# Kernel optimization log

Hardware: AMD Instinct MI355X
Metric: run time of the kernel (lower is better)

## Reference

```python
import jax, jax.numpy as jnp
import numpy as np

B, S, D, H = 2, 2048, 2048, 32
HD = D // H  # head_dim = 64
NEG = -1e10


def setup_inputs() -> dict:
    key = jax.random.key(0)
    k1, k2, k3 = jax.random.split(key, 3)
    hidden_states = jax.random.normal(k1, (B, S, D), dtype=jnp.float32)
    W = jax.random.normal(k2, (D, 3 * D), dtype=jnp.float32) * (1.0 / np.sqrt(D))
    b = jax.random.normal(k3, (3 * D,), dtype=jnp.float32) * 0.02
    return {"hidden_states": hidden_states, "W": W, "b": b}


def reference(hidden_states, W, b):
    # fused QKV projection: [B,S,D] @ [D,3D] -> [B,S,3D]
    qvk = hidden_states @ W + b
    # OPT interleaved layout: reshape to [B,S,D,3]; channel 0=q, 1=v, 2=k
    qvk = qvk.reshape(B, S, D, 3)
    q = qvk[..., 0].reshape(B, S, H, HD)
    v = qvk[..., 1].reshape(B, S, H, HD)
    k = qvk[..., 2].reshape(B, S, H, HD)
    # causal bias: -1e10 strictly above diagonal, shape [1,1,S,S]
    bias = jnp.triu(jnp.full((S, S), NEG, dtype=jnp.float32), 1)[None, None]
    # dot_product_attention_weights: scale q by 1/sqrt(head_dim)
    scale = jnp.asarray(1.0 / np.sqrt(HD), dtype=jnp.float32)
    scores = jnp.einsum('bqhd,bkhd->bhqk', q * scale, k) + bias  # [B,H,S,S]
    attn_weights = jax.nn.softmax(scores, axis=-1)
    attn_output = jnp.einsum('bhqk,bkhd->bqhd', attn_weights, v)  # [B,S,H,HD]
    return attn_output.reshape(B, S, D)
```

## Files before the change

kernel.cpp:

```cpp
#include <hip/hip_runtime.h>
#include <hip/hip_bf16.h>
#include <stdint.h>

typedef unsigned short ushort_t;
typedef __bf16 bf16x8 __attribute__((ext_vector_type(8)));
typedef float f32x4 __attribute__((ext_vector_type(4)));
typedef float f32x16 __attribute__((ext_vector_type(16)));
typedef int int4v __attribute__((ext_vector_type(4)));
typedef ushort_t ushort8 __attribute__((ext_vector_type(8)));

__device__ __forceinline__ ushort_t f2bf(float f) {
  union { float f; unsigned int u; } v; v.f = f;
  unsigned int r = v.u + 0x7fffu + ((v.u >> 16) & 1u);
  return (ushort_t)(r >> 16);
}

__device__ __forceinline__ bf16x8 ld_bf8(const ushort_t* p) {
  return *reinterpret_cast<const bf16x8*>(p);
}

__device__ __forceinline__ void g2lds16(const void* g, void* l) {
  __builtin_amdgcn_global_load_lds(
      (const __attribute__((address_space(1))) unsigned int*)g,
      (__attribute__((address_space(3))) unsigned int*)l,
      16, 0, 0);
}

__device__ __forceinline__ float ex2(float x) { return __builtin_amdgcn_exp2f(x); }

__device__ __forceinline__ int cvtpk(float a, float b) {
  int r;
  asm("v_cvt_pk_bf16_f32 %0, %1, %2" : "=v"(r) : "v"(a), "v"(b));
  return r;
}

__global__ __launch_bounds__(256) void cvt_hs(const float* __restrict__ in,
                                              ushort_t* __restrict__ out) {
  int i = (blockIdx.x * 256 + threadIdx.x) * 8;
  float4 a = *reinterpret_cast<const float4*>(in + i);
  float4 b = *reinterpret_cast<const float4*>(in + i + 4);
  ushort8 r;
  r[0] = f2bf(a.x); r[1] = f2bf(a.y); r[2] = f2bf(a.z); r[3] = f2bf(a.w);
  r[4] = f2bf(b.x); r[5] = f2bf(b.y); r[6] = f2bf(b.z); r[7] = f2bf(b.w);
  *reinterpret_cast<ushort8*>(out + i) = r;
}

__global__ __launch_bounds__(256) void transpose_W(const float* __restrict__ Win,
                                                   ushort_t* __restrict__ Wt) {
  __shared__ ushort_t T[64][65];
  const int t = threadIdx.x;
  const int k0 = (blockIdx.x & 31) * 64;
  const int n0 = (blockIdx.x >> 5) * 64;
#pragma unroll
  for (int i = 0; i < 16; ++i) {
    int idx = i * 256 + t;
    int r = idx >> 6, c = idx & 63;
    T[r][c] = f2bf(Win[(k0 + r) * 6144 + n0 + c]);
  }
  __syncthreads();
#pragma unroll
  for (int i = 0; i < 16; ++i) {
    int idx = i * 256 + t;
    int nr = idx >> 6, kc = idx & 63;
    Wt[(n0 + nr) * 2048 + k0 + kc] = T[kc][nr];
  }
}

__global__ __launch_bounds__(256, 2) void gemm_qkv(
    const ushort_t* __restrict__ A, const ushort_t* __restrict__ Bt,
    const float* __restrict__ bias,
    ushort_t* __restrict__ Qb, ushort_t* __restrict__ Kb,
    ushort_t* __restrict__ VT) {
  __shared__ __align__(16) char smem[40960];
  ushort_t* A0 = (ushort_t*)smem;
  ushort_t* A1 = (ushort_t*)(smem + 8192);
  ushort_t* B0 = (ushort_t*)(smem + 16384);
  ushort_t* B1 = (ushort_t*)(smem + 28672);
  ushort_t* Cs = (ushort_t*)smem;
  const int t = threadIdx.x;
  const int w = t >> 6, l = t & 63;
  const int lo = l & 15, hi = l >> 4;
  const int wr = w >> 1, wc = w & 1;

  int bid = blockIdx.x;
  int swz = (bid & 7) * 128 + (bid >> 3);
  const int mt = swz & 31, nt = swz >> 5;
  const int bm = mt * 128;
  const int bn = nt * 192;

  f32x4 acc[4][6];
#pragma unroll
  for (int i = 0; i < 4; ++i)
#pragma unroll
    for (int j = 0; j < 6; ++j) acc[i][j] = f32x4{0.f, 0.f, 0.f, 0.f};

  const ushort_t* Ag = A + (size_t)bm * 2048;
  const ushort_t* Bg = Bt + (size_t)bn * 2048;

#define STAGE(Ad, Bd, kk_)                                       \
  do {                                                           \
    for (int r2 = 0; r2 < 2; ++r2) {                             \
      int c_ = r2 * 256 + t;                                     \
      int row_ = c_ >> 2, s4_ = c_ & 3;                          \
      int slot_ = s4_ ^ ((row_ & 3) ^ ((row_ >> 2) & 3));        \
      g2lds16(Ag + row_ * 2048 + (kk_) + slot_ * 8, (Ad) + c_ * 8); \
    }                                                            \
    for (int r3 = 0; r3 < 3; ++r3) {                             \
      int c_ = r3 * 256 + t;                                     \
      int row_ = c_ >> 2, s4_ = c_ & 3;                          \
      int slot_ = s4_ ^ ((row_ & 3) ^ ((row_ >> 2) & 3));        \
      g2lds16(Bg + row_ * 2048 + (kk_) + slot_ * 8, (Bd) + c_ * 8); \
    }                                                            \
  } while (0)

  STAGE(A0, B0, 0);
  __syncthreads();
  ushort_t *Ac = A0, *Bc = B0, *An = A1, *Bn = B1;

  for (int kk = 0; kk < 2048; kk += 32) {
    if (kk + 32 < 2048) STAGE(An, Bn, kk + 32);
    bf16x8 af[4], bfr[6];
#pragma unroll
    for (int mf = 0; mf < 4; ++mf) {
      int row = wr * 64 + mf * 16 + lo;
      int fr = (row & 3) ^ ((row >> 2) & 3);
      af[mf] = ld_bf8(Ac + row * 32 + ((hi ^ fr) << 3));
    }
#pragma unroll
    for (int nf = 0; nf < 6; ++nf) {
      int row = wc * 96 + nf * 16 + lo;
      int fr = (row & 3) ^ ((row >> 2) & 3);
      bfr[nf] = ld_bf8(Bc + row * 32 + ((hi ^ fr) << 3));
    }
    __builtin_amdgcn_s_setprio(1);
#pragma unroll
    for (int mf = 0; mf < 4; ++mf)
#pragma unroll
      for (int nf = 0; nf < 6; ++nf)
        acc[mf][nf] = __builtin_amdgcn_mfma_f32_16x16x32_bf16(
            af[mf], bfr[nf], acc[mf][nf], 0, 0, 0);
    __builtin_amdgcn_s_setprio(0);
    __syncthreads();
    ushort_t* tmp;
    tmp = Ac; Ac = An; An = tmp;
    tmp = Bc; Bc = Bn; Bn = tmp;
  }
#undef STAGE

  float bv[6];
  int ch[6];
#pragma unroll
  for (int nf = 0; nf < 6; ++nf) {
    int nl = wc * 96 + nf * 16 + lo;
    bv[nf] = bias[bn + nl];
    ch[nf] = nl % 3;
  }
  const int b_ = bm >> 11;
  const int bh = (b_ << 5) + nt;
  const float QS = 0.125f * 1.44269504f;

#pragma unroll
  for (int h = 0; h < 2; ++h) {
    if (wr == h) {
#pragma unroll
      for (int mf = 0; mf < 4; ++mf)
#pragma unroll
        for (int nf = 0; nf < 6; ++nf) {
          int rloc = mf * 16 + hi * 4;
          int nl = wc * 96 + nf * 16 + lo;
          f32x4 a = acc[mf][nf];
#pragma unroll
          for (int j = 0; j < 4; ++j) {
            float v = a[j] + bv[nf];
            if (ch[nf] == 0) v *= QS;
            Cs[(rloc + j) * 200 + nl] = f2bf(v);
          }
        }
    }
    __syncthreads();
    const int sbase = (bm & 2047) + h * 64;
#pragma unroll
    for (int it = 0; it < 2; ++it) {
      int slot = it * 256 + t;
      int r = slot >> 3, g = slot & 7;
      ushort8 vq, vk;
#pragma unroll
      for (int u = 0; u < 8; ++u) {
        int hd = g * 8 + u;
        vq[u] = Cs[r * 200 + hd * 3];
        vk[u] = Cs[r * 200 + hd * 3 + 2];
      }
      size_t rowoff = ((size_t)bh * 2048 + sbase + r) * 64 + g * 8;
      *reinterpret_cast<ushort8*>(Qb + rowoff) = vq;
      *reinterpret_cast<ushort8*>(Kb + rowoff) = vk;
    }
#pragma unroll
    for (int it = 0; it < 2; ++it) {
      int slot = it * 256 + t;
      int hd = slot >> 3, sg = slot & 7;
      ushort8 vv;
#pragma unroll
      for (int u = 0; u < 8; ++u) vv[u] = Cs[(sg * 8 + u) * 200 + hd * 3 + 1];
      *reinterpret_cast<ushort8*>(VT + ((size_t)bh * 64 + hd) * 2048 + sbase +
                                  sg * 8) = vv;
    }
    __syncthreads();
  }
}

__global__ __launch_bounds__(64) void attn(
    const ushort_t* __restrict__ Qb, const ushort_t* __restrict__ Kb,
    const ushort_t* __restrict__ VT, float* __restrict__ out) {
  __shared__ float Ld[32 * 66];
  const int l = threadIdx.x;
  const int ql = l & 31, hi = l >> 5;

  const int bid = blockIdx.x;
  const int bh = bid & 63;
  const int qt = 63 - (bid >> 6);
  const int q0 = qt * 32;
  const int nch = qt + 1;

  const ushort_t* qp = Qb + (bh * 2048 + q0 + ql) * 64 + hi * 8;
  bf16x8 qf[4];
#pragma unroll
  for (int dc = 0; dc < 4; ++dc) qf[dc] = ld_bf8(qp + dc * 16);

  f32x16 o0, o1;
#pragma unroll
  for (int r = 0; r < 16; ++r) { o0[r] = 0.f; o1[r] = 0.f; }
  float mr = -1e30f, lr = 0.f;

  const ushort_t* kbase = Kb + bh * 2048 * 64 + hi * 8;
  const ushort_t* vbase = VT + (bh * 64 + ql) * 2048 + hi * 8;

  bf16x8 kf[4], vf0[2], vf1[2];
  {
    const ushort_t* kp = kbase + ql * 64;
#pragma unroll
    for (int dc = 0; dc < 4; ++dc) kf[dc] = ld_bf8(kp + dc * 16);
#pragma unroll
    for (int s = 0; s < 2; ++s) {
      const ushort_t* vp = vbase + s * 16;
      vf0[s] = ld_bf8(vp);
      vf1[s] = ld_bf8(vp + 32 * 2048);
    }
  }

  for (int c = 0; c < nch; ++c) {
    const int cn = (c + 1 < nch) ? (c + 1) : c;
    const ushort_t* kpn = kbase + (cn * 32 + ql) * 64;
    bf16x8 kn[4], vn0[2], vn1[2];
#pragma unroll
    for (int dc = 0; dc < 4; ++dc) kn[dc] = ld_bf8(kpn + dc * 16);
#pragma unroll
    for (int s = 0; s < 2; ++s) {
      const ushort_t* vpn = vbase + cn * 32 + s * 16;
      vn0[s] = ld_bf8(vpn);
      vn1[s] = ld_bf8(vpn + 32 * 2048);
    }

    f32x16 p;
#pragma unroll
    for (int r = 0; r < 16; ++r) p[r] = 0.f;
    __builtin_amdgcn_s_setprio(1);
#pragma unroll
    for (int dc = 0; dc < 4; ++dc)
      p = __builtin_amdgcn_mfma_f32_32x32x16_bf16(kf[dc], qf[dc], p, 0, 0, 0);
    __builtin_amdgcn_s_setprio(0);
    if (c == nch - 1) {
#pragma unroll
      for (int r = 0; r < 16; ++r) {
        int kvr = (r & 3) + 8 * (r >> 2) + 4 * hi;
        if (kvr > ql) p[r] = -1e30f;
      }
    }
    float a0 = fmaxf(p[0], p[1]), a1 = fmaxf(p[2], p[3]);
    float a2 = fmaxf(p[4], p[5]), a3 = fmaxf(p[6], p[7]);
    float a4 = fmaxf(p[8], p[9]), a5 = fmaxf(p[10], p[11]);
    float a6 = fmaxf(p[12], p[13]), a7 = fmaxf(p[14], p[15]);
    float mx = fmaxf(fmaxf(fmaxf(a0, a1), fmaxf(a2, a3)),
                     fmaxf(fmaxf(a4, a5), fmaxf(a6, a7)));
    if (__any(mx > mr + 10.0f)) {
      mx = fmaxf(mx, __shfl_xor(mx, 32));
      float mn = fmaxf(mr, mx);
      float scl = ex2(mr - mn);
      mr = mn;
      lr *= scl;
#pragma unroll
      for (int r = 0; r < 16; ++r) { o0[r] *= scl; o1[r] *= scl; }
    }
#pragma unroll
    for (int r = 0; r < 16; ++r) p[r] = ex2(p[r] - mr);
    float s0 = (p[0] + p[1]) + (p[2] + p[3]);
    float s1 = (p[4] + p[5]) + (p[6] + p[7]);
    float s2 = (p[8] + p[9]) + (p[10] + p[11]);
    float s3 = (p[12] + p[13]) + (p[14] + p[15]);
    lr += (s0 + s1) + (s2 + s3);

    __builtin_amdgcn_s_setprio(1);
#pragma unroll
    for (int s = 0; s < 2; ++s) {
      int x0 = cvtpk(p[8 * s + 0], p[8 * s + 1]);
      int x1 = cvtpk(p[8 * s + 2], p[8 * s + 3]);
      int y0 = cvtpk(p[8 * s + 4], p[8 * s + 5]);
      int y1 = cvtpk(p[8 * s + 6], p[8 * s + 7]);
      int ox0 = __shfl_xor(x0, 32);
      int ox1 = __shfl_xor(x1, 32);
      int oy0 = __shfl_xor(y0, 32);
      int oy1 = __shfl_xor(y1, 32);
      int4v wv;
      wv[0] = hi ? oy0 : x0;
      wv[1] = hi ? oy1 : x1;
      wv[2] = hi ? y0 : ox0;
      wv[3] = hi ? y1 : ox1;
      bf16x8 pf = __builtin_bit_cast(bf16x8, wv);
      o0 = __builtin_amdgcn_mfma_f32_32x32x16_bf16(vf0[s], pf, o0, 0, 0, 0);
      o1 = __builtin_amdgcn_mfma_f32_32x32x16_bf16(vf1[s], pf, o1, 0, 0, 0);
    }
    __builtin_amdgcn_s_setprio(0);
#pragma unroll
    for (int dc = 0; dc < 4; ++dc) kf[dc] = kn[dc];
#pragma unroll
    for (int s = 0; s < 2; ++s) {
      vf0[s] = vn0[s];
      vf1[s] = vn1[s];
    }
  }

  const float lrf = lr + __shfl_xor(lr, 32);
  const float inv = 1.0f / lrf;
#pragma unroll
  for (int r = 0; r < 16; ++r) {
    int hdv = (r & 3) + 8 * (r >> 2) + 4 * hi;
    Ld[ql * 66 + hdv] = o0[r] * inv;
    Ld[ql * 66 + 32 + hdv] = o1[r] * inv;
  }
  __syncthreads();
  const int b_ = bh >> 5, h = bh & 31;
  float* op = out + (size_t)(b_ * 2048 + q0) * 2048 + h * 64 + l;
#pragma unroll
  for (int i = 0; i < 32; ++i) {
    op[(size_t)i * 2048] = Ld[i * 66 + l];
  }
}

extern "C" void kernel_launch(void* const* d_in, const int* in_sizes, int n_in,
                              void* d_out, int out_size, void* d_ws,
                              size_t ws_size, hipStream_t stream) {
  (void)in_sizes; (void)n_in; (void)out_size; (void)ws_size;
  const float* hs = (const float*)d_in[0];
  const float* W = (const float*)d_in[1];
  const float* bias = (const float*)d_in[2];
  float* out = (float*)d_out;

  char* ws = (char*)d_ws;
  ushort_t* Abf = (ushort_t*)(ws);
  ushort_t* Wt = (ushort_t*)(ws + (16u << 20));
  ushort_t* Qb = (ushort_t*)(ws + (40u << 20));
  ushort_t* Kb = (ushort_t*)(ws + (56u << 20));
  ushort_t* VT = (ushort_t*)(ws + (72u << 20));

  hipLaunchKernelGGL(cvt_hs, dim3(4096), dim3(256), 0, stream, hs, Abf);
  hipLaunchKernelGGL(transpose_W, dim3(3072), dim3(256), 0, stream, W, Wt);
  hipLaunchKernelGGL(gemm_qkv, dim3(1024), dim3(256), 0, stream, Abf, Wt, bias,
                     Qb, Kb, VT);
  hipLaunchKernelGGL(attn, dim3(4096), dim3(64), 0, stream, Qb, Kb, VT, out);
}
```

Baseline: 263.4 us.

## Pair causal query tiles per block and double-buffer K/V loads in attention

Each attention block now processes two query tiles, pr and 63-pr, so every block does the same amount of causal work, and the grid is halved to 2048 blocks. The KV loop is unrolled by two with ping-pong register buffers (kA/kB). This removes the per-iteration register copies and the clamped redundant prefetch, and the diagonal mask now runs only on the last chunk. The cost is fewer blocks for latency hiding and tiles handled one after another inside a block. Register pressure may also rise from the doubled buffers.

After: 258.2 us. No clear change (-2.0%).

```diff
diff --git a/kernel.cpp b/kernel.cpp
--- a/kernel.cpp
+++ b/kernel.cpp
@@ -208,6 +208,84 @@
   }
 }
 
+__device__ __forceinline__ void ldkv(const ushort_t* kp, const ushort_t* vp,
+                                     bf16x8 k[4], bf16x8 v0[2], bf16x8 v1[2]) {
+#pragma unroll
+  for (int dc = 0; dc < 4; ++dc) k[dc] = ld_bf8(kp + dc * 16);
+#pragma unroll
+  for (int s = 0; s < 2; ++s) {
+    v0[s] = ld_bf8(vp + s * 16);
+    v1[s] = ld_bf8(vp + s * 16 + 32 * 2048);
+  }
+}
+
+__device__ __forceinline__ void proc_chunk(const bf16x8 kf[4],
+                                           const bf16x8 vf0[2],
+                                           const bf16x8 vf1[2],
+                                           const bf16x8 qf[4], f32x16& o0,
+                                           f32x16& o1, float& mr, float& lr,
+                                           bool diag, int ql, int hi) {
+  f32x16 p;
+#pragma unroll
+  for (int r = 0; r < 16; ++r) p[r] = 0.f;
+  __builtin_amdgcn_s_setprio(1);
+#pragma unroll
+  for (int dc = 0; dc < 4; ++dc)
+    p = __builtin_amdgcn_mfma_f32_32x32x16_bf16(kf[dc], qf[dc], p, 0, 0, 0);
+  __builtin_amdgcn_s_setprio(0);
+  if (diag) {
+#pragma unroll
+    for (int r = 0; r < 16; ++r) {
+      int kvr = (r & 3) + 8 * (r >> 2) + 4 * hi;
+      if (kvr > ql) p[r] = -1e30f;
+    }
+  }
+  float a0 = fmaxf(p[0], p[1]), a1 = fmaxf(p[2], p[3]);
+  float a2 = fmaxf(p[4], p[5]), a3 = fmaxf(p[6], p[7]);
+  float a4 = fmaxf(p[8], p[9]), a5 = fmaxf(p[10], p[11]);
+  float a6 = fmaxf(p[12], p[13]), a7 = fmaxf(p[14], p[15]);
+  float mx = fmaxf(fmaxf(fmaxf(a0, a1), fmaxf(a2, a3)),
+                   fmaxf(fmaxf(a4, a5), fmaxf(a6, a7)));
+  if (__any(mx > mr + 10.0f)) {
+    mx = fmaxf(mx, __shfl_xor(mx, 32));
+    float mn = fmaxf(mr, mx);
+    float scl = ex2(mr - mn);
+    mr = mn;
+    lr *= scl;
+#pragma unroll
+    for (int r = 0; r < 16; ++r) { o0[r] *= scl; o1[r] *= scl; }
+  }
+#pragma unroll
+  for (int r = 0; r < 16; ++r) p[r] = ex2(p[r] - mr);
+  float s0 = (p[0] + p[1]) + (p[2] + p[3]);
+  float s1 = (p[4] + p[5]) + (p[6] + p[7]);
+  float s2 = (p[8] + p[9]) + (p[10] + p[11]);
+  float s3 = (p[12] + p[13]) + (p[14] + p[15]);
+  lr += (s0 + s1) + (s2 + s3);
+
+  __builtin_amdgcn_s_setprio(1);
+#pragma unroll
+  for (int s = 0; s < 2; ++s) {
+    int x0 = cvtpk(p[8 * s + 0], p[8 * s + 1]);
+    int x1 = cvtpk(p[8 * s + 2], p[8 * s + 3]);
+    int y0 = cvtpk(p[8 * s + 4], p[8 * s + 5]);
+    int y1 = cvtpk(p[8 * s + 6], p[8 * s + 7]);
+    int ox0 = __shfl_xor(x0, 32);
+    int ox1 = __shfl_xor(x1, 32);
+    int oy0 = __shfl_xor(y0, 32);
+    int oy1 = __shfl_xor(y1, 32);
+    int4v wv;
+    wv[0] = hi ? oy0 : x0;
+    wv[1] = hi ? oy1 : x1;
+    wv[2] = hi ? y0 : ox0;
+    wv[3] = hi ? y1 : ox1;
+    bf16x8 pf = __builtin_bit_cast(bf16x8, wv);
+    o0 = __builtin_amdgcn_mfma_f32_32x32x16_bf16(vf0[s], pf, o0, 0, 0, 0);
+    o1 = __builtin_amdgcn_mfma_f32_32x32x16_bf16(vf1[s], pf, o1, 0, 0, 0);
+  }
+  __builtin_amdgcn_s_setprio(0);
+}
+
 __global__ __launch_bounds__(64) void attn(
     const ushort_t* __restrict__ Qb, const ushort_t* __restrict__ Kb,
     const ushort_t* __restrict__ VT, float* __restrict__ out) {
@@ -217,131 +295,66 @@
 
   const int bid = blockIdx.x;
   const int bh = bid & 63;
-  const int qt = 63 - (bid >> 6);
-  const int q0 = qt * 32;
-  const int nch = qt + 1;
-
-  const ushort_t* qp = Qb + (bh * 2048 + q0 + ql) * 64 + hi * 8;
-  bf16x8 qf[4];
-#pragma unroll
-  for (int dc = 0; dc < 4; ++dc) qf[dc] = ld_bf8(qp + dc * 16);
-
-  f32x16 o0, o1;
-#pragma unroll
-  for (int r = 0; r < 16; ++r) { o0[r] = 0.f; o1[r] = 0.f; }
-  float mr = -1e30f, lr = 0.f;
+  const int pr = bid >> 6;
+  const int b_ = bh >> 5, h = bh & 31;
 
   const ushort_t* kbase = Kb + bh * 2048 * 64 + hi * 8;
   const ushort_t* vbase = VT + (bh * 64 + ql) * 2048 + hi * 8;
-
-  bf16x8 kf[4], vf0[2], vf1[2];
-  {
+  const int KSTR = 32 * 64;
+  const int VSTR = 32;
+
+#pragma unroll 1
+  for (int tile = 0; tile < 2; ++tile) {
+    const int qt = tile ? (63 - pr) : pr;
+    const int q0 = qt * 32;
+    const int nch = qt + 1;
+
+    const ushort_t* qp = Qb + (bh * 2048 + q0 + ql) * 64 + hi * 8;
+    bf16x8 qf[4];
+#pragma unroll
+    for (int dc = 0; dc < 4; ++dc) qf[dc] = ld_bf8(qp + dc * 16);
+
+    f32x16 o0, o1;
+#pragma unroll
+    for (int r = 0; r < 16; ++r) { o0[r] = 0.f; o1[r] = 0.f; }
+    float mr = -1e30f, lr = 0.f;
+
+    bf16x8 kA[4], vA0[2], vA1[2], kB[4], vB0[2], vB1[2];
     const ushort_t* kp = kbase + ql * 64;
-#pragma unroll
-    for (int dc = 0; dc < 4; ++dc) kf[dc] = ld_bf8(kp + dc * 16);
-#pragma unroll
-    for (int s = 0; s < 2; ++s) {
-      const ushort_t* vp = vbase + s * 16;
-      vf0[s] = ld_bf8(vp);
-      vf1[s] = ld_bf8(vp + 32 * 2048);
-    }
-  }
-
-  for (int c = 0; c < nch; ++c) {
-    const int cn = (c + 1 < nch) ? (c + 1) : c;
-    const ushort_t* kpn = kbase + (cn * 32 + ql) * 64;
-    bf16x8 kn[4], vn0[2], vn1[2];
-#pragma unroll
-    for (int dc = 0; dc < 4; ++dc) kn[dc] = ld_bf8(kpn + dc * 16);
-#pragma unroll
-    for (int s = 0; s < 2; ++s) {
-      const ushort_t* vpn = vbase + cn * 32 + s * 16;
-      vn0[s] = ld_bf8(vpn);
-      vn1[s] = ld_bf8(vpn + 32 * 2048);
-    }
-
-    f32x16 p;
-#pragma unroll
-    for (int r = 0; r < 16; ++r) p[r] = 0.f;
-    __builtin_amdgcn_s_setprio(1);
-#pragma unroll
-    for (int dc = 0; dc < 4; ++dc)
-      p = __builtin_amdgcn_mfma_f32_32x32x16_bf16(kf[dc], qf[dc], p, 0, 0, 0);
-    __builtin_amdgcn_s_setprio(0);
-    if (c == nch - 1) {
-#pragma unroll
-      for (int r = 0; r < 16; ++r) {
-        int kvr = (r & 3) + 8 * (r >> 2) + 4 * hi;
-        if (kvr > ql) p[r] = -1e30f;
+    const ushort_t* vp = vbase;
+    ldkv(kp, vp, kA, vA0, vA1);
+
+    int c = 0;
+    while (c + 2 <= nch) {
+      kp += KSTR; vp += VSTR;
+      ldkv(kp, vp, kB, vB0, vB1);
+      proc_chunk(kA, vA0, vA1, qf, o0, o1, mr, lr, false, ql, hi);
+      if (c + 2 < nch) {
+        kp += KSTR; vp += VSTR;
+        ldkv(kp, vp, kA, vA0, vA1);
       }
-    }
-    float a0 = fmaxf(p[0], p[1]), a1 = fmaxf(p[2], p[3]);
-    float a2 = fmaxf(p[4], p[5]), a3 = fmaxf(p[6], p[7]);
-    float a4 = fmaxf(p[8], p[9]), a5 = fmaxf(p[10], p[11]);
-    float a6 = fmaxf(p[12], p[13]), a7 = fmaxf(p[14], p[15]);
-    float mx = fmaxf(fmaxf(fmaxf(a0, a1), fmaxf(a2, a3)),
-                     fmaxf(fmaxf(a4, a5), fmaxf(a6, a7)));
-    if (__any(mx > mr + 10.0f)) {
-      mx = fmaxf(mx, __shfl_xor(mx, 32));
-      float mn = fmaxf(mr, mx);
-      float scl = ex2(mr - mn);
-      mr = mn;
-      lr *= scl;
-#pragma unroll
-      for (int r = 0; r < 16; ++r) { o0[r] *= scl; o1[r] *= scl; }
-    }
-#pragma unroll
-    for (int r = 0; r < 16; ++r) p[r] = ex2(p[r] - mr);
-    float s0 = (p[0] + p[1]) + (p[2] + p[3]);
-    float s1 = (p[4] + p[5]) + (p[6] + p[7]);
-    float s2 = (p[8] + p[9]) + (p[10] + p[11]);
-    float s3 = (p[12] + p[13]) + (p[14] + p[15]);
-    lr += (s0 + s1) + (s2 + s3);
-
-    __builtin_amdgcn_s_setprio(1);
-#pragma unroll
-    for (int s = 0; s < 2; ++s) {
-      int x0 = cvtpk(p[8 * s + 0], p[8 * s + 1]);
-      int x1 = cvtpk(p[8 * s + 2], p[8 * s + 3]);
-      int y0 = cvtpk(p[8 * s + 4], p[8 * s + 5]);
-      int y1 = cvtpk(p[8 * s + 6], p[8 * s + 7]);
-      int ox0 = __shfl_xor(x0, 32);
-      int ox1 = __shfl_xor(x1, 32);
-      int oy0 = __shfl_xor(y0, 32);
-      int oy1 = __shfl_xor(y1, 32);
-      int4v wv;
-      wv[0] = hi ? oy0 : x0;
-      wv[1] = hi ? oy1 : x1;
-      wv[2] = hi ? y0 : ox0;
-      wv[3] = hi ? y1 : ox1;
-      bf16x8 pf = __builtin_bit_cast(bf16x8, wv);
-      o0 = __builtin_amdgcn_mfma_f32_32x32x16_bf16(vf0[s], pf, o0, 0, 0, 0);
-      o1 = __builtin_amdgcn_mfma_f32_32x32x16_bf16(vf1[s], pf, o1, 0, 0, 0);
-    }
-    __builtin_amdgcn_s_setprio(0);
-#pragma unroll
-    for (int dc = 0; dc < 4; ++dc) kf[dc] = kn[dc];
-#pragma unroll
-    for (int s = 0; s < 2; ++s) {
-      vf0[s] = vn0[s];
-      vf1[s] = vn1[s];
-    }
-  }
-
-  const float lrf = lr + __shfl_xor(lr, 32);
-  const float inv = 1.0f / lrf;
-#pragma unroll
-  for (int r = 0; r < 16; ++r) {
-    int hdv = (r & 3) + 8 * (r >> 2) + 4 * hi;
-    Ld[ql * 66 + hdv] = o0[r] * inv;
-    Ld[ql * 66 + 32 + hdv] = o1[r] * inv;
-  }
-  __syncthreads();
-  const int b_ = bh >> 5, h = bh & 31;
-  float* op = out + (size_t)(b_ * 2048 + q0) * 2048 + h * 64 + l;
-#pragma unroll
-  for (int i = 0; i < 32; ++i) {
-    op[(size_t)i * 2048] = Ld[i * 66 + l];
+      proc_chunk(kB, vB0, vB1, qf, o0, o1, mr, lr, (c + 1 == nch - 1), ql, hi);
+      c += 2;
+    }
+    if (c < nch) {
+      proc_chunk(kA, vA0, vA1, qf, o0, o1, mr, lr, true, ql, hi);
+    }
+
+    const float lrf = lr + __shfl_xor(lr, 32);
+    const float inv = 1.0f / lrf;
+#pragma unroll
+    for (int r = 0; r < 16; ++r) {
+      int hdv = (r & 3) + 8 * (r >> 2) + 4 * hi;
+      Ld[ql * 66 + hdv] = o0[r] * inv;
+      Ld[ql * 66 + 32 + hdv] = o1[r] * inv;
+    }
+    __syncthreads();
+    float* op = out + (size_t)(b_ * 2048 + q0) * 2048 + h * 64 + l;
+#pragma unroll
+    for (int i = 0; i < 32; ++i) {
+      op[(size_t)i * 2048] = Ld[i * 66 + l];
+    }
+    __syncthreads();
   }
 }
 
@@ -365,5 +378,5 @@
   hipLaunchKernelGGL(transpose_W, dim3(3072), dim3(256), 0, stream, W, Wt);
   hipLaunchKernelGGL(gemm_qkv, dim3(1024), dim3(256), 0, stream, Abf, Wt, bias,
                      Qb, Kb, VT);
-  hipLaunchKernelGGL(attn, dim3(4096), dim3(64), 0, stream, Qb, Kb, VT, out);
-}
+  hipLaunchKernelGGL(attn, dim3(2048), dim3(64), 0, stream, Qb, Kb, VT, out);
+}
```
